# Optimization experiments

Measured on AMD Instinct MI355X. Metric: run time of the kernel, lower is better.

## Reference

```python
import jax, jax.numpy as jnp
import numpy as np

NUM_HEADS = 12
DIM = 768
NV = 4  # number of views
EPS = 1e-6


def _ln(x, g, b):
    m = x.mean(-1, keepdims=True)
    v = ((x - m) ** 2).mean(-1, keepdims=True)
    return (x - m) / jnp.sqrt(v + EPS) * g + b


def setup_inputs() -> dict:
    key = jax.random.key(0)
    ks = jax.random.split(key, 10)
    B, N, C, H = 4, 256, DIM, NUM_HEADS
    Hid = 4 * C
    s = 0.02
    return {
        'X': jax.random.normal(ks[0], (B * NV, N, C), jnp.float32),
        'norm1_g': jnp.ones((C,), jnp.float32),
        'norm1_b': jnp.zeros((C,), jnp.float32),
        'qkv_w': jax.random.normal(ks[1], (NV, 3 * C, C), jnp.float32) * s,
        'proj_w': jax.random.normal(ks[2], (NV, C, C), jnp.float32) * s,
        'proj_b': jnp.zeros((NV, C), jnp.float32),
        'norm2_g': jnp.ones((NV, C), jnp.float32),
        'norm2_b': jnp.zeros((NV, C), jnp.float32),
        'fc1_w': jax.random.normal(ks[3], (NV, Hid, C), jnp.float32) * s,
        'fc1_b': jnp.zeros((NV, Hid), jnp.float32),
        'fc2_w': jax.random.normal(ks[4], (NV, C, Hid), jnp.float32) * s,
        'fc2_b': jnp.zeros((NV, C), jnp.float32),
        'query': jax.random.normal(ks[5], (1, 1, C), jnp.float32),
        'mha_in_w': jax.random.normal(ks[6], (NV, 3 * C, C), jnp.float32) * s,
        'mha_in_b': jnp.zeros((NV, 3 * C), jnp.float32),
        'mha_out_w': jax.random.normal(ks[7], (NV, C, C), jnp.float32) * s,
        'mha_out_b': jnp.zeros((NV, C), jnp.float32),
    }


def reference(X, norm1_g, norm1_b, qkv_w, proj_w, proj_b, norm2_g, norm2_b,
              fc1_w, fc1_b, fc2_w, fc2_b, query, mha_in_w, mha_in_b,
              mha_out_w, mha_out_b):
    B4, N, C = X.shape
    B = B4 // NV
    H = NUM_HEADS
    hd = C // H
    scale = hd ** -0.5

    Xv = X.reshape(B, NV, N, C)
    Xn = _ln(Xv, norm1_g, norm1_b)

    # ---- FusionAttention: 4x4 pairwise cross attention between views ----
    qkv = jnp.einsum('bvnc,vdc->vbnd', Xn, qkv_w)              # [V,B,N,3C]
    qkv = qkv.reshape(NV, B, N, 3, H, hd).transpose(3, 0, 1, 4, 2, 5)  # [3,V,B,H,N,hd]
    q, k, v = qkv[0], qkv[1], qkv[2]
    scores = jnp.einsum('ibhnd,jbhmd->ijbhnm', q, k) * scale   # [V,V,B,H,N,N]
    attn = jax.nn.softmax(scores, axis=-1)
    ctx = jnp.einsum('ijbhnm,jbhmd->ijbhnd', attn, v)
    ctx = ctx.transpose(0, 1, 2, 4, 3, 5).reshape(NV, NV, B, N, C)
    # proj_i is affine, so mean over j of proj(x_j) == proj(mean_j x_j)
    ctx_mean = ctx.mean(axis=1)                                # [V,B,N,C]
    xa = jnp.einsum('vbnc,voc->vbno', ctx_mean, proj_w) + proj_b[:, None, None, :]

    x = xa * 2.0
    h = _ln(x, norm2_g[:, None, None, :], norm2_b[:, None, None, :])
    h1 = jax.nn.gelu(jnp.einsum('vbnc,vhc->vbnh', h, fc1_w) + fc1_b[:, None, None, :],
                     approximate=False)
    h2 = jnp.einsum('vbnh,vch->vbnc', h1, fc2_w) + fc2_b[:, None, None, :]
    x = x + h2                                                  # [V,B,N,C]

    # ---- CrossAttentionWithLearnableQuery (query identical for all T,B) ----
    wq, wk, wv = jnp.split(mha_in_w, 3, axis=1)                 # each [V,C,C]
    bq, bk, bv = jnp.split(mha_in_b, 3, axis=1)                 # each [V,C]
    q0 = query.reshape(C)
    qh = (jnp.einsum('c,vdc->vd', q0, wq) + bq).reshape(NV, H, hd)
    kh = (jnp.einsum('vbnc,vdc->vbnd', x, wk) + bk[:, None, None, :]).reshape(NV, B, N, H, hd)
    vh = (jnp.einsum('vbnc,vdc->vbnd', x, wv) + bv[:, None, None, :]).reshape(NV, B, N, H, hd)
    s2 = jnp.einsum('vhd,vbnhd->vbhn', qh, kh) * scale
    a2 = jax.nn.softmax(s2, axis=-1)
    c2 = jnp.einsum('vbhn,vbnhd->vbhd', a2, vh).reshape(NV, B, C)
    o = jnp.einsum('vbc,voc->vbo', c2, mha_out_w) + mha_out_b[:, None, :]  # [V,B,C]
    o = o.transpose(1, 0, 2).reshape(B, NV * C)                 # concat views
    # every query position produces identical output -> broadcast over T=N
    return jnp.broadcast_to(o[:, None, :], (B, N, NV * C))
```

## Files before the change

kernel.cpp:

```cpp
#include <hip/hip_runtime.h>
#include <math.h>

#define NVIEW 4
#define BATCH 4
#define NSEQ  256
#define CDIM  768
#define HEADS 12
#define HD    64

typedef __attribute__((ext_vector_type(8))) short   short8;
typedef __attribute__((ext_vector_type(8))) unsigned short ushort8;
typedef __attribute__((ext_vector_type(4))) float   float4v;

typedef const __attribute__((address_space(1))) void gas_t;
typedef       __attribute__((address_space(3))) void las_t;

__device__ __forceinline__ unsigned short f2b(float x)
{
    union { float f; unsigned u; } c; c.f = x;
    unsigned r = (c.u + 0x7FFFu + ((c.u >> 16) & 1u)) >> 16;
    return (unsigned short)r;
}

__global__ void conv_bf16(const float* __restrict__ src, unsigned short* __restrict__ dst, int n)
{
    int idx = (blockIdx.x * 256 + threadIdx.x) * 8;
    if (idx >= n) return;
    float4 a = *(const float4*)(src + idx);
    float4 b = *(const float4*)(src + idx + 4);
    ushort8 o;
    o[0] = f2b(a.x); o[1] = f2b(a.y); o[2] = f2b(a.z); o[3] = f2b(a.w);
    o[4] = f2b(b.x); o[5] = f2b(b.y); o[6] = f2b(b.z); o[7] = f2b(b.w);
    *(ushort8*)(dst + idx) = o;
}

__device__ __forceinline__ void block_ln_row_b(const float* __restrict__ xrow,
                                               const float* __restrict__ g,
                                               const float* __restrict__ b,
                                               unsigned short* __restrict__ orow)
{
    const int t = threadIdx.x;
    float x0 = xrow[t], x1 = xrow[t + 256], x2 = xrow[t + 512];
    float s  = x0 + x1 + x2;
    float s2 = x0 * x0 + x1 * x1 + x2 * x2;
    #pragma unroll
    for (int off = 32; off > 0; off >>= 1) {
        s  += __shfl_down(s, off);
        s2 += __shfl_down(s2, off);
    }
    __shared__ float w1[4], w2[4];
    if ((t & 63) == 0) { w1[t >> 6] = s; w2[t >> 6] = s2; }
    __syncthreads();
    float S  = w1[0] + w1[1] + w1[2] + w1[3];
    float S2 = w2[0] + w2[1] + w2[2] + w2[3];
    float mean = S * (1.0f / 768.0f);
    float var  = S2 * (1.0f / 768.0f) - mean * mean;
    float inv  = rsqrtf(var + 1e-6f);
    orow[t]       = f2b((x0 - mean) * inv * g[t]       + b[t]);
    orow[t + 256] = f2b((x1 - mean) * inv * g[t + 256] + b[t + 256]);
    orow[t + 512] = f2b((x2 - mean) * inv * g[t + 512] + b[t + 512]);
}

__global__ void ln1_kernel(const float* __restrict__ X, const float* __restrict__ g,
                           const float* __restrict__ b, unsigned short* __restrict__ Xn)
{
    int rid = blockIdx.x;
    int n  = rid & 255;
    int bv = rid >> 8;
    int bb = bv >> 2, v = bv & 3;
    const float* xrow = X + (long)rid * CDIM;
    unsigned short* orow = Xn + ((long)(v * 4 + bb) * 256 + n) * CDIM;
    block_ln_row_b(xrow, g, b, orow);
}

__global__ void ln2_kernel(const float* __restrict__ Xin, const float* __restrict__ g,
                           const float* __restrict__ b, unsigned short* __restrict__ Out)
{
    int rid = blockIdx.x;
    int v = rid >> 10;
    const float* xrow = Xin + (long)rid * CDIM;
    block_ln_row_b(xrow, g + v * CDIM, b + v * CDIM, Out + (long)rid * CDIM);
}

template <int EPI, int TM, typename OT>
__launch_bounds__(256, 2)
__global__ void gemm_bf16(const unsigned short* __restrict__ A,
                          const unsigned short* __restrict__ W,
                          const float* __restrict__ bias, const float* __restrict__ resid,
                          OT* __restrict__ out, int M, int N, int K,
                          long wStride, long wOff, int bStride, int bOff)
{
    const int v = blockIdx.z;
    const unsigned short* Av = A + (long)v * M * K;
    const unsigned short* Wv = W + v * wStride + wOff;

    __shared__ unsigned short As[TM * 32];
    __shared__ unsigned short Bs[128 * 32];

    const int tid  = threadIdx.x;
    const int lane = tid & 63;
    const int wave = tid >> 6;
    const int l15  = lane & 15;
    const int quad = lane >> 4;
    const int row0 = blockIdx.y * TM, col0 = blockIdx.x * 128;

    constexpr int MI = (TM == 128) ? 4 : 4;
    constexpr int NI = (TM == 128) ? 4 : 2;
    const int mw = (TM == 128) ? (wave & 1) * 64 : 0;
    const int nw = (TM == 128) ? (wave >> 1) * 64 : wave * 32;

    float4v acc[MI][NI];
    #pragma unroll
    for (int i = 0; i < MI; ++i)
        #pragma unroll
        for (int j = 0; j < NI; ++j)
            acc[i][j] = (float4v){0.f, 0.f, 0.f, 0.f};

    const int rB = wave * 32 + (lane >> 2);
    const int rA = (TM == 128) ? rB : (wave * 16 + (lane >> 2));
    const int pA = lane & 3;

    for (int k0 = 0; k0 < K; k0 += 32) {
        __syncthreads();
        if constexpr (TM == 128) {
            #pragma unroll
            for (int g = 0; g < 2; ++g) {
                int r = rA + g * 16;
                int c = (pA - ((r >> 1) & 3)) & 3;
                const unsigned short* sa = Av + (long)(row0 + r) * K + k0 + c * 8;
                __builtin_amdgcn_global_load_lds((gas_t*)sa, (las_t*)&As[(wave * 32 + g * 16) * 32], 16, 0, 0);
            }
        } else {
            int r = rA;
            int c = (pA - ((r >> 1) & 3)) & 3;
            const unsigned short* sa = Av + (long)(row0 + r) * K + k0 + c * 8;
            __builtin_amdgcn_global_load_lds((gas_t*)sa, (las_t*)&As[(wave * 16) * 32], 16, 0, 0);
        }
        #pragma unroll
        for (int g = 0; g < 2; ++g) {
            int r = rB + g * 16;
            int c = (pA - ((r >> 1) & 3)) & 3;
            const unsigned short* sw = Wv + (long)(col0 + r) * K + k0 + c * 8;
            __builtin_amdgcn_global_load_lds((gas_t*)sw, (las_t*)&Bs[(wave * 32 + g * 16) * 32], 16, 0, 0);
        }
        __syncthreads();

        short8 af[MI], bfr[NI];
        #pragma unroll
        for (int mi = 0; mi < MI; ++mi) {
            int m = mw + mi * 16 + l15;
            int p = (quad + ((m >> 1) & 3)) & 3;
            af[mi] = *(const short8*)&As[m * 32 + p * 8];
        }
        #pragma unroll
        for (int ni = 0; ni < NI; ++ni) {
            int n = nw + ni * 16 + l15;
            int p = (quad + ((n >> 1) & 3)) & 3;
            bfr[ni] = *(const short8*)&Bs[n * 32 + p * 8];
        }
        #pragma unroll
        for (int mi = 0; mi < MI; ++mi)
            #pragma unroll
            for (int ni = 0; ni < NI; ++ni)
                acc[mi][ni] = __builtin_amdgcn_mfma_f32_16x16x32_bf16(af[mi], bfr[ni], acc[mi][ni], 0, 0, 0);
    }

    #pragma unroll
    for (int mi = 0; mi < MI; ++mi) {
        #pragma unroll
        for (int ni = 0; ni < NI; ++ni) {
            int rowb = row0 + mw + mi * 16 + quad * 4;
            int col  = col0 + nw + ni * 16 + l15;
            float bval = 0.f;
            if (EPI >= 1) bval = bias[v * bStride + bOff + col];
            #pragma unroll
            for (int r = 0; r < 4; ++r) {
                float x = acc[mi][ni][r] + bval;
                long off = (long)v * M * N + (long)(rowb + r) * N + col;
                if constexpr (EPI == 2) {
                    x = 0.5f * x * (1.0f + erff(x * 0.70710678118654752f));
                } else if constexpr (EPI == 3) {
                    x += resid[off];
                } else if constexpr (EPI == 4) {
                    x *= 2.0f;
                }
                if constexpr (sizeof(OT) == 2) ((unsigned short*)out)[off] = f2b(x);
                else                           ((float*)out)[off] = x;
            }
        }
    }
}

__launch_bounds__(256, 2)
__global__ void fusion_attn_mfma(const unsigned short* __restrict__ QKV,
                                 unsigned short* __restrict__ ctx)
{
    const int qt = blockIdx.x;
    const int b  = blockIdx.y / HEADS;
    const int h  = blockIdx.y % HEADS;
    const int i  = blockIdx.z;
    const int tid  = threadIdx.x;
    const int lane = tid & 63;
    const int wave = tid >> 6;
    const int l15  = lane & 15;
    const int quad = lane >> 4;

    __shared__ unsigned short Qs[64 * 72];
    __shared__ unsigned short Ks[128 * 64];
    __shared__ unsigned short Ps[64 * 136];
    __shared__ unsigned short Vt[64 * 136];

    {
        int r = tid >> 2, p16 = (tid & 3) * 16;
        const unsigned short* src = QKV + ((long)((i * 4 + b) * 256 + qt * 64 + r)) * 2304 + h * 64 + p16;
        *(ushort8*)(&Qs[r * 72 + p16])     = *(const ushort8*)(src);
        *(ushort8*)(&Qs[r * 72 + p16 + 8]) = *(const ushort8*)(src + 8);
    }

    float4v acc_o[4];
    #pragma unroll
    for (int e = 0; e < 4; ++e) acc_o[e] = (float4v){0.f, 0.f, 0.f, 0.f};

    for (int j = 0; j < 4; ++j) {
        const unsigned short* Kb = QKV + ((long)((j * 4 + b) * 256)) * 2304 + 768 + h * 64;
        const unsigned short* Vb = Kb + 768;

        float4v sacc[16];
        #pragma unroll
        for (int t = 0; t < 16; ++t) sacc[t] = (float4v){0.f, 0.f, 0.f, 0.f};

        for (int half = 0; half < 2; ++half) {
            __syncthreads();
            #pragma unroll
            for (int g = 0; g < 4; ++g) {
                int R = wave * 32 + g * 8;
                int r = R + (lane >> 3);
                int p = lane & 7;
                int c = (p - (r & 7)) & 7;
                const unsigned short* src = Kb + (long)(half * 128 + r) * 2304 + c * 8;
                __builtin_amdgcn_global_load_lds((gas_t*)src, (las_t*)&Ks[R * 64], 16, 0, 0);
            }
            __syncthreads();
            #pragma unroll
            for (int ks = 0; ks < 2; ++ks) {
                int lcq = ks * 4 + quad;
                short8 qf = *(const short8*)&Qs[(wave * 16 + l15) * 72 + lcq * 8];
                #pragma unroll
                for (int nn = 0; nn < 8; ++nn) {
                    int n = nn * 16 + l15;
                    int p = (lcq + (n & 7)) & 7;
                    short8 kf = *(const short8*)&Ks[n * 64 + p * 8];
                    sacc[half * 8 + nn] =
                        __builtin_amdgcn_mfma_f32_16x16x32_bf16(qf, kf, sacc[half * 8 + nn], 0, 0, 0);
                }
            }
        }

        float rmax[4] = {-1e30f, -1e30f, -1e30f, -1e30f};
        #pragma unroll
        for (int t = 0; t < 16; ++t)
            #pragma unroll
            for (int r = 0; r < 4; ++r)
                rmax[r] = fmaxf(rmax[r], sacc[t][r] * 0.125f);
        #pragma unroll
        for (int off = 1; off < 16; off <<= 1)
            #pragma unroll
            for (int r = 0; r < 4; ++r)
                rmax[r] = fmaxf(rmax[r], __shfl_xor(rmax[r], off));
        float rsum[4] = {0.f, 0.f, 0.f, 0.f};
        #pragma unroll
        for (int t = 0; t < 16; ++t)
            #pragma unroll
            for (int r = 0; r < 4; ++r) {
                float e = __expf(sacc[t][r] * 0.125f - rmax[r]);
                sacc[t][r] = e;
                rsum[r] += e;
            }
        #pragma unroll
        for (int off = 1; off < 16; off <<= 1)
            #pragma unroll
            for (int r = 0; r < 4; ++r)
                rsum[r] += __shfl_xor(rsum[r], off);
        float invl[4];
        #pragma unroll
        for (int r = 0; r < 4; ++r) invl[r] = 1.0f / rsum[r];

        float4v pv[4];
        #pragma unroll
        for (int e = 0; e < 4; ++e) pv[e] = (float4v){0.f, 0.f, 0.f, 0.f};

        for (int half = 0; half < 2; ++half) {
            __syncthreads();
            #pragma unroll
            for (int nn = 0; nn < 8; ++nn)
                #pragma unroll
                for (int r = 0; r < 4; ++r)
                    Ps[(wave * 16 + quad * 4 + r) * 136 + nn * 16 + l15] = f2b(sacc[half * 8 + nn][r]);
            {
                int n = tid & 127;
                int c0 = (tid >> 7) * 4;
                #pragma unroll
                for (int cc = 0; cc < 4; ++cc) {
                    int c = c0 + cc;
                    ushort8 vv = *(const ushort8*)(Vb + (long)(half * 128 + n) * 2304 + c * 8);
                    #pragma unroll
                    for (int jj = 0; jj < 8; ++jj)
                        Vt[(c * 8 + jj) * 136 + n] = vv[jj];
                }
            }
            __syncthreads();
            #pragma unroll
            for (int ks = 0; ks < 4; ++ks) {
                int lc = ks * 4 + quad;
                short8 pf = *(const short8*)&Ps[(wave * 16 + l15) * 136 + lc * 8];
                #pragma unroll
                for (int et = 0; et < 4; ++et) {
                    short8 vf = *(const short8*)&Vt[(et * 16 + l15) * 136 + lc * 8];
                    pv[et] = __builtin_amdgcn_mfma_f32_16x16x32_bf16(pf, vf, pv[et], 0, 0, 0);
                }
            }
        }
        #pragma unroll
        for (int et = 0; et < 4; ++et)
            #pragma unroll
            for (int r = 0; r < 4; ++r)
                acc_o[et][r] += pv[et][r] * invl[r];
    }

    #pragma unroll
    for (int et = 0; et < 4; ++et)
        #pragma unroll
        for (int r = 0; r < 4; ++r) {
            int row = (i * 4 + b) * 256 + qt * 64 + wave * 16 + quad * 4 + r;
            int col = h * 64 + et * 16 + l15;
            ctx[(long)row * 768 + col] = f2b(acc_o[et][r] * 0.25f);
        }
}

__global__ void qh_kernel(const float* __restrict__ query, const float* __restrict__ Win,
                          const float* __restrict__ Bin, float* __restrict__ QH)
{
    int gid = blockIdx.x * 256 + threadIdx.x;
    int v = gid / 768, d = gid - v * 768;
    const float* w = Win + ((long)v * 2304 + d) * 768;
    float s = 0.f;
    for (int c = 0; c < 768; c += 4) {
        float4 w4 = *(const float4*)(w + c);
        float4 q4 = *(const float4*)(query + c);
        s += q4.x * w4.x + q4.y * w4.y + q4.z * w4.z + q4.w * w4.w;
    }
    QH[gid] = s + Bin[(long)v * 2304 + d];
}

__launch_bounds__(256, 2)
__global__ void cross_attn(const float* __restrict__ KVH, const float* __restrict__ QH,
                           float* __restrict__ C2)
{
    const int h = blockIdx.x, b = blockIdx.y, v = blockIdx.z;
    const int t = threadIdx.x;
    __shared__ float qv[64];
    __shared__ float p[256];
    __shared__ float part[4][64];
    __shared__ float wred[4], wred2[4];

    if (t < 64) qv[t] = QH[(v * 12 + h) * 64 + t];
    __syncthreads();

    const float* krow = KVH + ((long)((v * 4 + b) * 256 + t)) * 1536 + h * 64;
    float s = 0.f;
    #pragma unroll
    for (int e = 0; e < 64; e += 4) {
        float4 k4 = *(const float4*)(krow + e);
        s += qv[e] * k4.x + qv[e + 1] * k4.y + qv[e + 2] * k4.z + qv[e + 3] * k4.w;
    }
    s *= 0.125f;
    float m4 = s;
    #pragma unroll
    for (int off = 32; off > 0; off >>= 1) m4 = fmaxf(m4, __shfl_down(m4, off));
    if ((t & 63) == 0) wred[t >> 6] = m4;
    __syncthreads();
    float rmax = fmaxf(fmaxf(wred[0], wred[1]), fmaxf(wred[2], wred[3]));
    float ev = __expf(s - rmax);
    p[t] = ev;
    float s4 = ev;
    #pragma unroll
    for (int off = 32; off > 0; off >>= 1) s4 += __shfl_down(s4, off);
    if ((t & 63) == 0) wred2[t >> 6] = s4;
    __syncthreads();
    float inv = 1.0f / (wred2[0] + wred2[1] + wred2[2] + wred2[3]);

    const int e = t & 63, ch = t >> 6;
    const float* vbase = KVH + ((long)((v * 4 + b) * 256)) * 1536 + 768 + h * 64 + e;
    float accv = 0.f;
    for (int m = ch * 64; m < ch * 64 + 64; ++m)
        accv += p[m] * vbase[(long)m * 1536];
    part[ch][e] = accv;
    __syncthreads();
    if (t < 64)
        C2[(v * 4 + b) * 768 + h * 64 + t] =
            (part[0][t] + part[1][t] + part[2][t] + part[3][t]) * inv;
}

__launch_bounds__(256, 4)
__global__ void out_matvec(const float* __restrict__ C2, const float* __restrict__ Wout,
                           const float* __restrict__ Bout, float* __restrict__ obc)
{
    const int bi   = blockIdx.x;
    const int v    = bi / 192;
    const int dblk = bi - v * 192;
    const int t    = threadIdx.x;
    const int wave = t >> 6;
    const int lane = t & 63;
    const int d    = dblk * 4 + wave;

    __shared__ float c2s[3072];
    #pragma unroll
    for (int idx = 0; idx < 3072; idx += 256) c2s[idx + t] = C2[v * 3072 + idx + t];
    __syncthreads();

    const float* w = Wout + ((long)v * 768 + d) * 768;
    float acc0 = 0.f, acc1 = 0.f, acc2 = 0.f, acc3 = 0.f;
    #pragma unroll
    for (int k = 0; k < 3; ++k) {
        int c = k * 256 + lane * 4;
        float4 w4 = *(const float4*)(w + c);
        float4 a0 = *(const float4*)&c2s[c];
        float4 a1 = *(const float4*)&c2s[768 + c];
        float4 a2 = *(const float4*)&c2s[1536 + c];
        float4 a3 = *(const float4*)&c2s[2304 + c];
        acc0 += w4.x * a0.x + w4.y * a0.y + w4.z * a0.z + w4.w * a0.w;
        acc1 += w4.x * a1.x + w4.y * a1.y + w4.z * a1.z + w4.w * a1.w;
        acc2 += w4.x * a2.x + w4.y * a2.y + w4.z * a2.z + w4.w * a2.w;
        acc3 += w4.x * a3.x + w4.y * a3.y + w4.z * a3.z + w4.w * a3.w;
    }
    #pragma unroll
    for (int off = 32; off > 0; off >>= 1) {
        acc0 += __shfl_down(acc0, off);
        acc1 += __shfl_down(acc1, off);
        acc2 += __shfl_down(acc2, off);
        acc3 += __shfl_down(acc3, off);
    }
    if (lane == 0) {
        float bb = Bout[v * 768 + d];
        obc[0 * 3072 + v * 768 + d] = acc0 + bb;
        obc[1 * 3072 + v * 768 + d] = acc1 + bb;
        obc[2 * 3072 + v * 768 + d] = acc2 + bb;
        obc[3 * 3072 + v * 768 + d] = acc3 + bb;
    }
}

__launch_bounds__(256, 4)
__global__ void out_bcast(const float* __restrict__ obc, float* __restrict__ out)
{
    const int b  = blockIdx.x >> 6;
    const int n0 = (blockIdx.x & 63) * 4;
    const int t  = threadIdx.x;
    const float4* src = (const float4*)(obc + (long)b * 3072);
    float4 v0 = src[t], v1 = src[t + 256], v2 = src[t + 512];
    float4* dst = (float4*)(out + ((long)(b * 256 + n0)) * 3072);
    #pragma unroll
    for (int r = 0; r < 4; ++r) {
        dst[r * 768 + t]       = v0;
        dst[r * 768 + t + 256] = v1;
        dst[r * 768 + t + 512] = v2;
    }
}

extern "C" void kernel_launch(void* const* d_in, const int* in_sizes, int n_in,
                              void* d_out, int out_size, void* d_ws, size_t ws_size,
                              hipStream_t stream)
{
    const float* X        = (const float*)d_in[0];
    const float* n1g      = (const float*)d_in[1];
    const float* n1b      = (const float*)d_in[2];
    const float* qkv_w    = (const float*)d_in[3];
    const float* proj_w   = (const float*)d_in[4];
    const float* proj_b   = (const float*)d_in[5];
    const float* n2g      = (const float*)d_in[6];
    const float* n2b      = (const float*)d_in[7];
    const float* fc1_w    = (const float*)d_in[8];
    const float* fc1_b    = (const float*)d_in[9];
    const float* fc2_w    = (const float*)d_in[10];
    const float* fc2_b    = (const float*)d_in[11];
    const float* query    = (const float*)d_in[12];
    const float* mha_in_w = (const float*)d_in[13];
    const float* mha_in_b = (const float*)d_in[14];
    const float* mha_out_w= (const float*)d_in[15];
    const float* mha_out_b= (const float*)d_in[16];
    float* out = (float*)d_out;

    char* wsb = (char*)d_ws;
    unsigned short* wbuf = (unsigned short*)wsb;
    unsigned short* rgA  = (unsigned short*)(wsb + 18874368);
    char*           rgB  = wsb + 25165824;
    float*          xbuf = (float*)(wsb + 50331648);
    float*          qh   = (float*)(wsb + 62914560);
    float*          c2   = (float*)(wsb + 62926848);
    float*          obc  = (float*)(wsb + 62976000);

    unsigned short* QKV = (unsigned short*)rgB;
    unsigned short* H1  = (unsigned short*)rgB;
    float*          KVH = (float*)rgB;

    conv_bf16<<<3456, 256, 0, stream>>>(qkv_w, wbuf, 7077888);
    ln1_kernel<<<4096, 256, 0, stream>>>(X, n1g, n1b, rgA);
    gemm_bf16<0, 128, unsigned short><<<dim3(18, 8, 4), 256, 0, stream>>>(
        rgA, wbuf, nullptr, nullptr, QKV, 1024, 2304, 768, 2304L * 768, 0, 0, 0);
    fusion_attn_mfma<<<dim3(4, 48, 4), 256, 0, stream>>>(QKV, rgA);
    conv_bf16<<<1152, 256, 0, stream>>>(proj_w, wbuf, 2359296);
    gemm_bf16<4, 64, float><<<dim3(6, 16, 4), 256, 0, stream>>>(
        rgA, wbuf, proj_b, nullptr, xbuf, 1024, 768, 768, 768L * 768, 0, 768, 0);
    ln2_kernel<<<4096, 256, 0, stream>>>(xbuf, n2g, n2b, rgA);
    conv_bf16<<<4608, 256, 0, stream>>>(fc1_w, wbuf, 9437184);
    gemm_bf16<2, 128, unsigned short><<<dim3(24, 8, 4), 256, 0, stream>>>(
        rgA, wbuf, fc1_b, nullptr, H1, 1024, 3072, 768, 3072L * 768, 0, 3072, 0);
    conv_bf16<<<4608, 256, 0, stream>>>(fc2_w, wbuf, 9437184);
    gemm_bf16<3, 64, unsigned short><<<dim3(6, 16, 4), 256, 0, stream>>>(
        H1, wbuf, fc2_b, xbuf, rgA, 1024, 768, 3072, 768L * 3072, 0, 768, 0);
    conv_bf16<<<3456, 256, 0, stream>>>(mha_in_w, wbuf, 7077888);
    gemm_bf16<1, 64, float><<<dim3(12, 16, 4), 256, 0, stream>>>(
        rgA, wbuf, mha_in_b, nullptr, KVH, 1024, 1536, 768, 2304L * 768, 768L * 768, 2304, 768);
    qh_kernel<<<12, 256, 0, stream>>>(query, mha_in_w, mha_in_b, qh);
    cross_attn<<<dim3(12, 4, 4), 256, 0, stream>>>(KVH, qh, c2);
    out_matvec<<<768, 256, 0, stream>>>(c2, mha_out_w, mha_out_b, obc);
    out_bcast<<<256, 256, 0, stream>>>(obc, out);
}
```

Before: 480.2 us.

## Double GEMM K-tile to 64 with XOR swizzle; parallelize qh matvec per wave

The bf16 GEMM now stages 64-wide K slices in LDS instead of 32, using an XOR-based swizzle for the new 128-byte rows. This halves the number of barrier pairs per K loop and issues two MFMA sub-steps per tile. It doubles LDS use per block, which may reduce occupancy. Separately, the query projection matvec, which previously ran on 12 blocks with one serial thread per output, now uses 768 blocks with one wave per output row, the query cached in LDS, and a shuffle reduction.

```diff
diff --git a/kernel.cpp b/kernel.cpp
--- a/kernel.cpp
+++ b/kernel.cpp
@@ -94,8 +94,8 @@
     const unsigned short* Av = A + (long)v * M * K;
     const unsigned short* Wv = W + v * wStride + wOff;
 
-    __shared__ unsigned short As[TM * 32];
-    __shared__ unsigned short Bs[128 * 32];
+    __shared__ unsigned short As[TM * 64];
+    __shared__ unsigned short Bs[128 * 64];
 
     const int tid  = threadIdx.x;
     const int lane = tid & 63;
@@ -104,7 +104,7 @@
     const int quad = lane >> 4;
     const int row0 = blockIdx.y * TM, col0 = blockIdx.x * 128;
 
-    constexpr int MI = (TM == 128) ? 4 : 4;
+    constexpr int MI = 4;
     constexpr int NI = (TM == 128) ? 4 : 2;
     const int mw = (TM == 128) ? (wave & 1) * 64 : 0;
     const int nw = (TM == 128) ? (wave >> 1) * 64 : wave * 32;
@@ -116,53 +116,50 @@
         for (int j = 0; j < NI; ++j)
             acc[i][j] = (float4v){0.f, 0.f, 0.f, 0.f};
 
-    const int rB = wave * 32 + (lane >> 2);
-    const int rA = (TM == 128) ? rB : (wave * 16 + (lane >> 2));
-    const int pA = lane & 3;
-
-    for (int k0 = 0; k0 < K; k0 += 32) {
+    const int lr8 = lane >> 3;
+    const int p8  = lane & 7;
+
+    for (int k0 = 0; k0 < K; k0 += 64) {
         __syncthreads();
-        if constexpr (TM == 128) {
-            #pragma unroll
-            for (int g = 0; g < 2; ++g) {
-                int r = rA + g * 16;
-                int c = (pA - ((r >> 1) & 3)) & 3;
-                const unsigned short* sa = Av + (long)(row0 + r) * K + k0 + c * 8;
-                __builtin_amdgcn_global_load_lds((gas_t*)sa, (las_t*)&As[(wave * 32 + g * 16) * 32], 16, 0, 0);
-            }
-        } else {
-            int r = rA;
-            int c = (pA - ((r >> 1) & 3)) & 3;
+        #pragma unroll
+        for (int g = 0; g < TM / 32; ++g) {
+            int G = wave * (TM / 32) + g;
+            int r = G * 8 + lr8;
+            int c = p8 ^ (r & 7);
             const unsigned short* sa = Av + (long)(row0 + r) * K + k0 + c * 8;
-            __builtin_amdgcn_global_load_lds((gas_t*)sa, (las_t*)&As[(wave * 16) * 32], 16, 0, 0);
-        }
-        #pragma unroll
-        for (int g = 0; g < 2; ++g) {
-            int r = rB + g * 16;
-            int c = (pA - ((r >> 1) & 3)) & 3;
+            __builtin_amdgcn_global_load_lds((gas_t*)sa, (las_t*)&As[G * 512], 16, 0, 0);
+        }
+        #pragma unroll
+        for (int g = 0; g < 4; ++g) {
+            int G = wave * 4 + g;
+            int r = G * 8 + lr8;
+            int c = p8 ^ (r & 7);
             const unsigned short* sw = Wv + (long)(col0 + r) * K + k0 + c * 8;
-            __builtin_amdgcn_global_load_lds((gas_t*)sw, (las_t*)&Bs[(wave * 32 + g * 16) * 32], 16, 0, 0);
+            __builtin_amdgcn_global_load_lds((gas_t*)sw, (las_t*)&Bs[G * 512], 16, 0, 0);
         }
         __syncthreads();
 
-        short8 af[MI], bfr[NI];
-        #pragma unroll
-        for (int mi = 0; mi < MI; ++mi) {
-            int m = mw + mi * 16 + l15;
-            int p = (quad + ((m >> 1) & 3)) & 3;
-            af[mi] = *(const short8*)&As[m * 32 + p * 8];
-        }
-        #pragma unroll
-        for (int ni = 0; ni < NI; ++ni) {
-            int n = nw + ni * 16 + l15;
-            int p = (quad + ((n >> 1) & 3)) & 3;
-            bfr[ni] = *(const short8*)&Bs[n * 32 + p * 8];
-        }
-        #pragma unroll
-        for (int mi = 0; mi < MI; ++mi)
-            #pragma unroll
-            for (int ni = 0; ni < NI; ++ni)
-                acc[mi][ni] = __builtin_amdgcn_mfma_f32_16x16x32_bf16(af[mi], bfr[ni], acc[mi][ni], 0, 0, 0);
+        #pragma unroll
+        for (int ks = 0; ks < 2; ++ks) {
+            short8 af[MI], bfr[NI];
+            #pragma unroll
+            for (int mi = 0; mi < MI; ++mi) {
+                int m = mw + mi * 16 + l15;
+                int p = (ks * 4 + quad) ^ (m & 7);
+                af[mi] = *(const short8*)&As[m * 64 + p * 8];
+            }
+            #pragma unroll
+            for (int ni = 0; ni < NI; ++ni) {
+                int n = nw + ni * 16 + l15;
+                int p = (ks * 4 + quad) ^ (n & 7);
+                bfr[ni] = *(const short8*)&Bs[n * 64 + p * 8];
+            }
+            #pragma unroll
+            for (int mi = 0; mi < MI; ++mi)
+                #pragma unroll
+                for (int ni = 0; ni < NI; ++ni)
+                    acc[mi][ni] = __builtin_amdgcn_mfma_f32_16x16x32_bf16(af[mi], bfr[ni], acc[mi][ni], 0, 0, 0);
+        }
     }
 
     #pragma unroll
@@ -337,19 +334,35 @@
         }
 }
 
+__launch_bounds__(256, 4)
 __global__ void qh_kernel(const float* __restrict__ query, const float* __restrict__ Win,
                           const float* __restrict__ Bin, float* __restrict__ QH)
 {
-    int gid = blockIdx.x * 256 + threadIdx.x;
-    int v = gid / 768, d = gid - v * 768;
+    const int bi   = blockIdx.x;
+    const int v    = bi / 192;
+    const int dblk = bi - v * 192;
+    const int t    = threadIdx.x;
+    const int wave = t >> 6;
+    const int lane = t & 63;
+    const int d    = dblk * 4 + wave;
+
+    __shared__ float qs[768];
+    for (int idx = t; idx < 768; idx += 256) qs[idx] = query[idx];
+    __syncthreads();
+
     const float* w = Win + ((long)v * 2304 + d) * 768;
-    float s = 0.f;
-    for (int c = 0; c < 768; c += 4) {
+    float acc = 0.f;
+    #pragma unroll
+    for (int k = 0; k < 3; ++k) {
+        int c = k * 256 + lane * 4;
         float4 w4 = *(const float4*)(w + c);
-        float4 q4 = *(const float4*)(query + c);
-        s += q4.x * w4.x + q4.y * w4.y + q4.z * w4.z + q4.w * w4.w;
-    }
-    QH[gid] = s + Bin[(long)v * 2304 + d];
+        float4 q4 = *(const float4*)&qs[c];
+        acc += w4.x * q4.x + w4.y * q4.y + w4.z * q4.z + w4.w * q4.w;
+    }
+    #pragma unroll
+    for (int off = 32; off > 0; off >>= 1) acc += __shfl_down(acc, off);
+    if (lane == 0)
+        QH[v * 768 + d] = acc + Bin[(long)v * 2304 + d];
 }
 
 __launch_bounds__(256, 2)
@@ -520,7 +533,7 @@
     conv_bf16<<<3456, 256, 0, stream>>>(mha_in_w, wbuf, 7077888);
     gemm_bf16<1, 64, float><<<dim3(12, 16, 4), 256, 0, stream>>>(
         rgA, wbuf, mha_in_b, nullptr, KVH, 1024, 1536, 768, 2304L * 768, 768L * 768, 2304, 768);
-    qh_kernel<<<12, 256, 0, stream>>>(query, mha_in_w, mha_in_b, qh);
+    qh_kernel<<<768, 256, 0, stream>>>(query, mha_in_w, mha_in_b, qh);
     cross_attn<<<dim3(12, 4, 4), 256, 0, stream>>>(KVH, qh, c2);
     out_matvec<<<768, 256, 0, stream>>>(c2, mha_out_w, mha_out_b, obc);
     out_bcast<<<256, 256, 0, stream>>>(obc, out);
```

Measured after the change: 447.1 us. 6.9% less time.
